# Optimization experiments

Measured on AMD Instinct MI355X. Metric: run time of the kernel, lower is better.

Reference implementation:

```python
import jax, jax.numpy as jnp
import numpy as np

H = 64   # hidden size
V = 29   # vocab / feature size
SOS = 27 # start-token index set to 1 in the initial one-hot


def _cell(x, h, c, Wih, Whh, bih, bhh):
    # PyTorch LSTMCell gate order: i, f, g, o
    g = x @ Wih.T + h @ Whh.T + bih + bhh
    i, f, gg, o = jnp.split(g, 4, axis=-1)
    c = jax.nn.sigmoid(f) * c + jax.nn.sigmoid(i) * jnp.tanh(gg)
    h = jax.nn.sigmoid(o) * jnp.tanh(c)
    return h, c


def setup_inputs() -> dict:
    key = jax.random.key(0)
    ks = iter(jax.random.split(key, 32))
    T, B = 1024, 512
    def p(shape, scale=0.05):
        return jax.random.normal(next(ks), shape, dtype=jnp.float32) * scale
    inp = {"input_seq": jax.random.normal(next(ks), (T, B, V), dtype=jnp.float32)}
    inp.update(
        enc_Wih0=p((4 * H, V)), enc_Whh0=p((4 * H, H)), enc_bih0=p((4 * H,)), enc_bhh0=p((4 * H,)),
        enc_Wih1=p((4 * H, H)), enc_Whh1=p((4 * H, H)), enc_bih1=p((4 * H,)), enc_bhh1=p((4 * H,)),
        d1_Wih=p((4 * H, V)), d1_Whh=p((4 * H, H)), d1_bih=p((4 * H,)), d1_bhh=p((4 * H,)),
        d2_Wih=p((4 * H, H)), d2_Whh=p((4 * H, H)), d2_bih=p((4 * H,)), d2_bhh=p((4 * H,)),
        cls_W=p((V, H)), cls_b=p((V,)),
    )
    return inp


def reference(input_seq, enc_Wih0, enc_Whh0, enc_bih0, enc_bhh0,
              enc_Wih1, enc_Whh1, enc_bih1, enc_bhh1,
              d1_Wih, d1_Whh, d1_bih, d1_bhh,
              d2_Wih, d2_Whh, d2_bih, d2_bhh,
              cls_W, cls_b):
    T, B, _ = input_seq.shape
    dt = input_seq.dtype
    z = jnp.zeros((B, H), dt)

    def layer(x_seq, Wih, Whh, bih, bhh):
        def step(carry, x):
            h, c = _cell(x, carry[0], carry[1], Wih, Whh, bih, bhh)
            return (h, c), h
        (h, c), ys = jax.lax.scan(step, (z, z), x_seq)
        return ys, h, c

    # 2-layer encoder LSTM with zero initial state
    y1, _, _ = layer(input_seq, enc_Wih0, enc_Whh0, enc_bih0, enc_bhh0)
    _, h1, c1 = layer(y1, enc_Wih1, enc_Whh1, enc_bih1, enc_bhh1)  # top-layer final (h, c)

    let0 = jnp.zeros((B, V), dt).at[:, SOS].set(1.0)

    def dec_step(carry, _):
        h1, c1, h2, c2, let = carry
        h1, c1 = _cell(let, h1, c1, d1_Wih, d1_Whh, d1_bih, d1_bhh)
        h2, c2 = _cell(h1, h2, c2, d2_Wih, d2_Whh, d2_bih, d2_bhh)
        pred = h2 @ cls_W.T + cls_b  # [B, V]
        idx = jnp.argmax(pred, axis=-1)  # [B]
        # Faithful to original bug: sets column idx[b] to 1 for ALL rows, for each b
        let = jnp.zeros((B, V), pred.dtype).at[:, idx].set(1.0)
        return (h1, c1, h2, c2, let), pred

    _, outputs = jax.lax.scan(dec_step, (h1, c1, z, z, let0), None, length=T)
    return outputs  # [T, B, V]
```

## Files before the change

kernel.cpp:

```cpp
#include <hip/hip_runtime.h>
#include <math.h>

#define TSTEPS 1024
#define BATCH  512
#define HID    64
#define VOC    29
#define SOS    27
#define MASK29 0x1FFFFFFFu

#define ENC_BLOCKS 256
#define DEC_BLOCKS 256
#define NTHREADS   512
#define WMAX       16

__device__ __forceinline__ float frcp(float x){ return __builtin_amdgcn_rcpf(x); }
__device__ __forceinline__ float sigmf(float x){ return frcp(1.0f + __expf(-x)); }
__device__ __forceinline__ float tanhfast(float x){ return 1.0f - 2.0f*frcp(1.0f + __expf(2.0f*x)); }

__global__ __attribute__((amdgpu_flat_work_group_size(NTHREADS,NTHREADS), amdgpu_waves_per_eu(2,2)))
void enc_kernel(const float* __restrict__ x,
                const float* __restrict__ Wih0, const float* __restrict__ Whh0,
                const float* __restrict__ bih0, const float* __restrict__ bhh0,
                const float* __restrict__ Wih1, const float* __restrict__ Whh1,
                const float* __restrict__ bih1, const float* __restrict__ bhh1,
                float* __restrict__ h1g, float* __restrict__ c1g)
{
  const int tid = threadIdx.x;
  const int b0  = blockIdx.x * 2;
  const bool g0 = tid < 256;
  const int  r  = g0 ? tid : (tid-256);

  __shared__ __align__(16) float xs[2][32];
  __shared__ __align__(16) float h0s[2][HID], h1s[2][HID];
  __shared__ __align__(16) float gA[2][256], gB[2][256];

  float wh[64], w2[64];
  if (g0){
    #pragma unroll
    for (int k=0;k<64;k++) wh[k] = Whh0[r*64+k];
    #pragma unroll
    for (int k=0;k<29;k++) w2[k] = Wih0[r*29+k];
    #pragma unroll
    for (int k=29;k<64;k++) w2[k] = 0.f;
  } else {
    #pragma unroll
    for (int k=0;k<64;k++){ wh[k] = Whh1[r*64+k]; w2[k] = Wih1[r*64+k]; }
  }
  const float bias = g0 ? (bih0[r]+bhh0[r]) : (bih1[r]+bhh1[r]);

  float creg = 0.f;
  if (tid < 128){ int u=tid>>6,k=tid&63; h0s[u][k]=0.f; h1s[u][k]=0.f; }

  const int pidx = tid - 448;
  const bool pf  = (pidx >= 0) && (pidx < 2*VOC);
  const int prow = pf ? (pidx/VOC) : 0;
  const int pcol = pf ? (pidx%VOC) : 0;
  if (pf) xs[prow][pcol] = x[(size_t)(b0+prow)*VOC + pcol];
  __syncthreads();

  for (int t=0;t<=TSTEPS;t++){
    float xv = 0.f;
    if (pf && t+1 < TSTEPS)
      xv = x[(size_t)(t+1)*BATCH*VOC + (size_t)(b0+prow)*VOC + pcol];

    if (g0){
      if (t < TSTEPS){
        #pragma unroll
        for (int u=0;u<2;u++){
          float a0=bias,a1=0.f,a2=0.f,a3=0.f;
          const float4* xv4 = (const float4*)xs[u];
          #pragma unroll
          for (int c=0;c<7;c++){
            float4 q=xv4[c];
            a0=fmaf(q.x,w2[4*c+0],a0); a1=fmaf(q.y,w2[4*c+1],a1);
            a2=fmaf(q.z,w2[4*c+2],a2); a3=fmaf(q.w,w2[4*c+3],a3);
          }
          a0=fmaf(xs[u][28],w2[28],a0);
          const float4* h4=(const float4*)h0s[u];
          #pragma unroll
          for (int c=0;c<16;c++){
            float4 q=h4[c];
            a0=fmaf(q.x,wh[4*c+0],a0); a1=fmaf(q.y,wh[4*c+1],a1);
            a2=fmaf(q.z,wh[4*c+2],a2); a3=fmaf(q.w,wh[4*c+3],a3);
          }
          gA[u][r]=(a0+a1)+(a2+a3);
        }
      }
    } else {
      if (t >= 1){
        #pragma unroll
        for (int u=0;u<2;u++){
          float a0=bias,a1=0.f,a2=0.f,a3=0.f;
          const float4* i4=(const float4*)h0s[u];
          const float4* h4=(const float4*)h1s[u];
          #pragma unroll
          for (int c=0;c<16;c++){
            float4 q=i4[c], w=h4[c];
            a0=fmaf(q.x,w2[4*c+0],a0); a1=fmaf(q.y,w2[4*c+1],a1);
            a2=fmaf(q.z,w2[4*c+2],a2); a3=fmaf(q.w,w2[4*c+3],a3);
            a0=fmaf(w.x,wh[4*c+0],a0); a1=fmaf(w.y,wh[4*c+1],a1);
            a2=fmaf(w.z,wh[4*c+2],a2); a3=fmaf(w.w,wh[4*c+3],a3);
          }
          gB[u][r]=(a0+a1)+(a2+a3);
        }
      }
    }
    __syncthreads();
    if (tid < 128){
      if (t < TSTEPS){
        int u=tid>>6,k=tid&63;
        float ig=gA[u][k],fg=gA[u][64+k],gg=gA[u][128+k],og=gA[u][192+k];
        float c=sigmf(fg)*creg + sigmf(ig)*tanhfast(gg);
        creg=c; h0s[u][k]=sigmf(og)*tanhfast(c);
      }
    } else if (tid < 384){
      if (t >= 1){
        int tt=tid-256,u=tt>>6,k=tt&63;
        float ig=gB[u][k],fg=gB[u][64+k],gg=gB[u][128+k],og=gB[u][192+k];
        float c=sigmf(fg)*creg + sigmf(ig)*tanhfast(gg);
        creg=c; h1s[u][k]=sigmf(og)*tanhfast(c);
      }
    }
    if (pf && t+1 < TSTEPS) xs[prow][pcol] = xv;
    __syncthreads();
  }

  if (tid >= 256 && tid < 384){
    int tt=tid-256,u=tt>>6,k=tt&63;
    h1g[(b0+u)*HID+k]=h1s[u][k];
    c1g[(b0+u)*HID+k]=creg;
  }
}

__global__ __attribute__((amdgpu_flat_work_group_size(NTHREADS,NTHREADS), amdgpu_waves_per_eu(2,2)))
void dec_kernel(const float* __restrict__ h1gp, const float* __restrict__ c1gp,
                const float* __restrict__ W1ih, const float* __restrict__ W1hh,
                const float* __restrict__ b1ih, const float* __restrict__ b1hh,
                const float* __restrict__ W2ih, const float* __restrict__ W2hh,
                const float* __restrict__ b2ih, const float* __restrict__ b2hh,
                const float* __restrict__ clsW, const float* __restrict__ clsb,
                float* __restrict__ out,
                unsigned long long* __restrict__ mseq)
{
  const int tid  = threadIdx.x;
  const int p    = tid & 1;
  const int r    = tid >> 1;
  const int q    = r & 3;
  const int m    = tid >> 3;
  const int g    = q*64 + m;
  const int blk  = blockIdx.x;
  const int b0   = blk * 2;

  __shared__ __align__(16) float clsW_s[VOC][68];
  __shared__ __align__(16) float clsb_s[32];
  __shared__ __align__(16) float h1s[2][2][HID], h2s[2][2][HID];
  __shared__ __align__(16) float h1ck[WMAX][2][HID], c1ck[WMAX][2][HID];
  __shared__ __align__(16) float h2ck[WMAX][2][HID], c2ck[WMAX][2][HID];
  __shared__ unsigned u_lds[WMAX];

  for (int i=tid;i<VOC*HID;i+=NTHREADS) clsW_s[i/HID][i%HID] = clsW[i];
  if (tid<VOC) clsb_s[tid]=clsb[tid];

  float w1h[32], w2i[32], w2h[32], wi1c[15];
  #pragma unroll
  for (int k=0;k<32;k++){
    w1h[k]=W1hh[g*HID+32*p+k];
    w2i[k]=W2ih[g*HID+32*p+k];
    w2h[k]=W2hh[g*HID+32*p+k];
  }
  const int cbase = p ? 15 : 0;
  const int cn    = p ? 14 : 15;
  #pragma unroll
  for (int j=0;j<15;j++) wi1c[j] = (j<cn) ? W1ih[g*VOC+cbase+j] : 0.f;
  const float biasg = p ? 0.f : (b1ih[g]+b1hh[g]);
  const float bias2 = p ? 0.f : (b2ih[g]+b2hh[g]);

  float c1r[2], c2r[2];
  c1r[0]=c1gp[(b0+0)*HID+m]; c1r[1]=c1gp[(b0+1)*HID+m];
  c2r[0]=0.f; c2r[1]=0.f;
  if (tid<128){
    int u=tid>>6,k=tid&63;
    h1s[0][u][k]=h1gp[(b0+u)*HID+k];
    h2s[0][u][k]=0.f;
  }
  __syncthreads();

  unsigned F = 1u<<SOS;
  int f = 0;
  unsigned rr = 0;
  int Wcur = 4, streak = 0;
  int pb = 0;

  while (f < TSTEPS){
    const int Wr = (TSTEPS - f < Wcur) ? (TSTEPS - f) : Wcur;
    const unsigned tag = rr + 1u;
    unsigned long long* __restrict__ mrow = mseq + (size_t)(rr&1u)*(WMAX*256);

    if (tid < Wr) u_lds[tid] = 0u;

    float it0 = biasg;
    #pragma unroll
    for (int jj=0;jj<15;jj++) it0 += ((F>>(cbase+jj))&1u) ? wi1c[jj] : 0.f;

    for (int j=0;j<Wr;j++){
      float h1n[2];
      #pragma unroll
      for (int u=0;u<2;u++){
        float a0=it0,a1=0.f,a2=0.f,a3=0.f;
        const float4* h4=(const float4*)(&h1s[pb][u][32*p]);
        #pragma unroll
        for (int c=0;c<8;c++){
          float4 qv=h4[c];
          a0=fmaf(qv.x,w1h[4*c+0],a0); a1=fmaf(qv.y,w1h[4*c+1],a1);
          a2=fmaf(qv.z,w1h[4*c+2],a2); a3=fmaf(qv.w,w1h[4*c+3],a3);
        }
        float v=(a0+a1)+(a2+a3);
        v += __shfl_xor(v,1);
        float x2=__shfl_xor(v,2), x4=__shfl_xor(v,4), x6=__shfl_xor(v,6);
        float ig = q==0?v : q==1?x2 : q==2?x4 : x6;
        float fg = q==1?v : q==0?x2 : q==3?x4 : x6;
        float gg = q==2?v : q==3?x2 : q==0?x4 : x6;
        float og = q==3?v : q==2?x2 : q==1?x4 : x6;
        float c = sigmf(fg)*c1r[u] + sigmf(ig)*tanhfast(gg);
        c1r[u]=c; h1n[u]=sigmf(og)*tanhfast(c);
      }
      if ((tid&7)==0){
        h1s[pb^1][0][m]=h1n[0]; h1s[pb^1][1][m]=h1n[1];
        h1ck[j][0][m]=h1n[0];   h1ck[j][1][m]=h1n[1];
        c1ck[j][0][m]=c1r[0];   c1ck[j][1][m]=c1r[1];
      }
      __syncthreads();

      float h2n[2];
      #pragma unroll
      for (int u=0;u<2;u++){
        float a0=bias2,a1=0.f,a2=0.f,a3=0.f;
        const float4* i4=(const float4*)(&h1s[pb^1][u][32*p]);
        const float4* h4=(const float4*)(&h2s[pb][u][32*p]);
        #pragma unroll
        for (int c=0;c<8;c++){
          float4 qv=i4[c], wv=h4[c];
          a0=fmaf(qv.x,w2i[4*c+0],a0); a1=fmaf(qv.y,w2i[4*c+1],a1);
          a2=fmaf(qv.z,w2i[4*c+2],a2); a3=fmaf(qv.w,w2i[4*c+3],a3);
          a0=fmaf(wv.x,w2h[4*c+0],a0); a1=fmaf(wv.y,w2h[4*c+1],a1);
          a2=fmaf(wv.z,w2h[4*c+2],a2); a3=fmaf(wv.w,w2h[4*c+3],a3);
        }
        float v=(a0+a1)+(a2+a3);
        v += __shfl_xor(v,1);
        float x2=__shfl_xor(v,2), x4=__shfl_xor(v,4), x6=__shfl_xor(v,6);
        float ig = q==0?v : q==1?x2 : q==2?x4 : x6;
        float fg = q==1?v : q==0?x2 : q==3?x4 : x6;
        float gg = q==2?v : q==3?x2 : q==0?x4 : x6;
        float og = q==3?v : q==2?x2 : q==1?x4 : x6;
        float c = sigmf(fg)*c2r[u] + sigmf(ig)*tanhfast(gg);
        c2r[u]=c; h2n[u]=sigmf(og)*tanhfast(c);
      }
      if ((tid&7)==0){
        h2s[pb^1][0][m]=h2n[0]; h2s[pb^1][1][m]=h2n[1];
        h2ck[j][0][m]=h2n[0];   h2ck[j][1][m]=h2n[1];
        c2ck[j][0][m]=c2r[0];   c2ck[j][1][m]=c2r[1];
      }
      __syncthreads();

      if (tid<64){
        const int s = f + j;
        int row=tid>>5, v=tid&31;
        float pv = -INFINITY;
        if (v<VOC){
          float a0=clsb_s[v],a1=0.f,a2=0.f,a3=0.f;
          const float4* h4=(const float4*)h2s[pb^1][row];
          #pragma unroll
          for (int c=0;c<16;c++){
            float4 qv=h4[c];
            a0=fmaf(qv.x,clsW_s[v][4*c+0],a0); a1=fmaf(qv.y,clsW_s[v][4*c+1],a1);
            a2=fmaf(qv.z,clsW_s[v][4*c+2],a2); a3=fmaf(qv.w,clsW_s[v][4*c+3],a3);
          }
          pv=(a0+a1)+(a2+a3);
          out[((size_t)s*BATCH + (size_t)(b0+row))*VOC + v]=pv;
        }
        int ix=v;
        #pragma unroll
        for (int off=16; off>0; off>>=1){
          float ov=__shfl_xor(pv,off);
          int   oi=__shfl_xor(ix,off);
          if (ov>pv || (ov==pv && oi<ix)){ pv=ov; ix=oi; }
        }
        unsigned bit = 1u<<ix;
        unsigned mb  = bit | __shfl_xor(bit,32);
        if (tid==0)
          __hip_atomic_store(&mrow[j*256+blk],
                             ((unsigned long long)tag<<32) | (unsigned long long)mb,
                             __ATOMIC_RELAXED, __HIP_MEMORY_SCOPE_AGENT);
      }
      pb ^= 1;
    }

    for (int w=tid; w<Wr*256; w+=NTHREADS){
      const int jj = w>>8, bb = w&255;
      unsigned long long vv;
      do {
        vv = __hip_atomic_load(&mrow[jj*256+bb], __ATOMIC_RELAXED, __HIP_MEMORY_SCOPE_AGENT);
      } while ((unsigned)(vv>>32) != tag);
      unsigned um = (unsigned)vv & MASK29;
      um |= __shfl_xor(um,1);  um |= __shfl_xor(um,2);  um |= __shfl_xor(um,4);
      um |= __shfl_xor(um,8);  um |= __shfl_xor(um,16); um |= __shfl_xor(um,32);
      if ((tid&63)==0) atomicOr(&u_lds[jj], um);
    }
    __syncthreads();

    int jstar = Wr;
    for (int jj=1;jj<Wr;jj++){ if (u_lds[jj-1]!=F){ jstar=jj; break; } }

    if (jstar==Wr){
      F = u_lds[Wr-1]; f += Wr; rr++;
      streak++;
      if (streak>=2 && Wcur<WMAX) Wcur*=2;
    } else {
      const int jm = jstar-1;
      c1r[0]=c1ck[jm][0][m]; c1r[1]=c1ck[jm][1][m];
      c2r[0]=c2ck[jm][0][m]; c2r[1]=c2ck[jm][1][m];
      if (tid<128){
        int u=tid>>6,k=tid&63;
        h1s[0][u][k]=h1ck[jm][u][k];
        h2s[0][u][k]=h2ck[jm][u][k];
      }
      pb = 0;
      F = u_lds[jm]; f += jstar; rr++;
      streak = 0; Wcur = jstar;
    }
    __syncthreads();
  }
}

extern "C" void kernel_launch(void* const* d_in, const int* in_sizes, int n_in,
                              void* d_out, int out_size, void* d_ws, size_t ws_size,
                              hipStream_t stream)
{
  const float* x     = (const float*)d_in[0];
  const float* eWih0 = (const float*)d_in[1];
  const float* eWhh0 = (const float*)d_in[2];
  const float* ebih0 = (const float*)d_in[3];
  const float* ebhh0 = (const float*)d_in[4];
  const float* eWih1 = (const float*)d_in[5];
  const float* eWhh1 = (const float*)d_in[6];
  const float* ebih1 = (const float*)d_in[7];
  const float* ebhh1 = (const float*)d_in[8];
  const float* d1Wih = (const float*)d_in[9];
  const float* d1Whh = (const float*)d_in[10];
  const float* d1bih = (const float*)d_in[11];
  const float* d1bhh = (const float*)d_in[12];
  const float* d2Wih = (const float*)d_in[13];
  const float* d2Whh = (const float*)d_in[14];
  const float* d2bih = (const float*)d_in[15];
  const float* d2bhh = (const float*)d_in[16];
  const float* clsW  = (const float*)d_in[17];
  const float* clsb  = (const float*)d_in[18];
  float* out = (float*)d_out;

  float* h1g = (float*)d_ws;
  float* c1g = h1g + BATCH*HID;
  unsigned long long* mseq =
      (unsigned long long*)((char*)d_ws + (size_t)(2*BATCH*HID)*sizeof(float));

  hipMemsetAsync(mseq, 0, (size_t)2*WMAX*256*sizeof(unsigned long long), stream);

  enc_kernel<<<ENC_BLOCKS, NTHREADS, 0, stream>>>(
      x, eWih0,eWhh0,ebih0,ebhh0, eWih1,eWhh1,ebih1,ebhh1, h1g,c1g);

  void* args[] = { (void*)&h1g, (void*)&c1g,
                   (void*)&d1Wih,(void*)&d1Whh,(void*)&d1bih,(void*)&d1bhh,
                   (void*)&d2Wih,(void*)&d2Whh,(void*)&d2bih,(void*)&d2bhh,
                   (void*)&clsW,(void*)&clsb,(void*)&out,
                   (void*)&mseq };
  hipLaunchCooperativeKernel((void*)dec_kernel, dim3(DEC_BLOCKS), dim3(NTHREADS),
                             args, 0, stream);
}
```

Baseline: 4.874 ms.

## Fuse encoder gate activation into matvec threads via shuffles, double-buffer state

The encoder kernel remaps threads so each quad of lanes holds the i/f/g/o rows for one hidden unit, exchanges the gate pre-activations with warp shuffles, and computes the cell update in place. This drops the gate LDS arrays and one of the two barriers per timestep. h and x buffers are double-buffered so the next step's reads don't race with writes. Every thread now evaluates the activation transcendentals redundantly, and the cell state is replicated four times.

```diff
diff --git a/kernel.cpp b/kernel.cpp
--- a/kernel.cpp
+++ b/kernel.cpp
@@ -28,107 +28,113 @@
   const int tid = threadIdx.x;
   const int b0  = blockIdx.x * 2;
   const bool g0 = tid < 256;
-  const int  r  = g0 ? tid : (tid-256);
-
-  __shared__ __align__(16) float xs[2][32];
-  __shared__ __align__(16) float h0s[2][HID], h1s[2][HID];
-  __shared__ __align__(16) float gA[2][256], gB[2][256];
-
-  float wh[64], w2[64];
+  const int  t2 = g0 ? tid : (tid-256);
+  const int  q  = t2 & 3;
+  const int  m  = t2 >> 2;
+  const int  g  = q*64 + m;
+
+  __shared__ __align__(16) float xs[2][2][32];
+  __shared__ __align__(16) float h0s[2][2][HID], h1s[2][2][HID];
+
+  float wa[64], wb[64];
+  float bias;
   if (g0){
     #pragma unroll
-    for (int k=0;k<64;k++) wh[k] = Whh0[r*64+k];
-    #pragma unroll
-    for (int k=0;k<29;k++) w2[k] = Wih0[r*29+k];
-    #pragma unroll
-    for (int k=29;k<64;k++) w2[k] = 0.f;
+    for (int k=0;k<29;k++) wa[k]=Wih0[g*29+k];
+    #pragma unroll
+    for (int k=29;k<64;k++) wa[k]=0.f;
+    #pragma unroll
+    for (int k=0;k<64;k++) wb[k]=Whh0[g*64+k];
+    bias = bih0[g]+bhh0[g];
   } else {
     #pragma unroll
-    for (int k=0;k<64;k++){ wh[k] = Whh1[r*64+k]; w2[k] = Wih1[r*64+k]; }
-  }
-  const float bias = g0 ? (bih0[r]+bhh0[r]) : (bih1[r]+bhh1[r]);
-
-  float creg = 0.f;
-  if (tid < 128){ int u=tid>>6,k=tid&63; h0s[u][k]=0.f; h1s[u][k]=0.f; }
-
-  const int pidx = tid - 448;
-  const bool pf  = (pidx >= 0) && (pidx < 2*VOC);
-  const int prow = pf ? (pidx/VOC) : 0;
-  const int pcol = pf ? (pidx%VOC) : 0;
-  if (pf) xs[prow][pcol] = x[(size_t)(b0+prow)*VOC + pcol];
+    for (int k=0;k<64;k++){ wa[k]=Wih1[g*64+k]; wb[k]=Whh1[g*64+k]; }
+    bias = bih1[g]+bhh1[g];
+  }
+
+  float creg[2]={0.f,0.f};
+  float hn[2]={0.f,0.f};
+
+  if (tid<256){ ((float*)h0s)[tid]=0.f; ((float*)h1s)[tid]=0.f; }
+  const int lrow = tid/29, lcol = tid - lrow*29;
+  const bool ldr = g0 && (tid<58);
+  if (ldr) xs[0][lrow][lcol] = x[(size_t)(b0+lrow)*VOC + lcol];
   __syncthreads();
 
+  int pb=0;
+  const bool q0=(q==0), q1=(q==1), q2=(q==2), q3=(q==3);
+
   for (int t=0;t<=TSTEPS;t++){
-    float xv = 0.f;
-    if (pf && t+1 < TSTEPS)
-      xv = x[(size_t)(t+1)*BATCH*VOC + (size_t)(b0+prow)*VOC + pcol];
+    float xv=0.f;
+    if (ldr && t+1<TSTEPS)
+      xv = x[(size_t)(t+1)*BATCH*VOC + (size_t)(b0+lrow)*VOC + lcol];
 
     if (g0){
-      if (t < TSTEPS){
+      if (t<TSTEPS){
         #pragma unroll
         for (int u=0;u<2;u++){
           float a0=bias,a1=0.f,a2=0.f,a3=0.f;
-          const float4* xv4 = (const float4*)xs[u];
+          const float4* xv4=(const float4*)xs[pb][u];
           #pragma unroll
           for (int c=0;c<7;c++){
-            float4 q=xv4[c];
-            a0=fmaf(q.x,w2[4*c+0],a0); a1=fmaf(q.y,w2[4*c+1],a1);
-            a2=fmaf(q.z,w2[4*c+2],a2); a3=fmaf(q.w,w2[4*c+3],a3);
+            float4 qv=xv4[c];
+            a0=fmaf(qv.x,wa[4*c+0],a0); a1=fmaf(qv.y,wa[4*c+1],a1);
+            a2=fmaf(qv.z,wa[4*c+2],a2); a3=fmaf(qv.w,wa[4*c+3],a3);
           }
-          a0=fmaf(xs[u][28],w2[28],a0);
-          const float4* h4=(const float4*)h0s[u];
+          a0=fmaf(xs[pb][u][28],wa[28],a0);
+          const float4* h4=(const float4*)h0s[pb][u];
           #pragma unroll
           for (int c=0;c<16;c++){
-            float4 q=h4[c];
-            a0=fmaf(q.x,wh[4*c+0],a0); a1=fmaf(q.y,wh[4*c+1],a1);
-            a2=fmaf(q.z,wh[4*c+2],a2); a3=fmaf(q.w,wh[4*c+3],a3);
+            float4 qv=h4[c];
+            a0=fmaf(qv.x,wb[4*c+0],a0); a1=fmaf(qv.y,wb[4*c+1],a1);
+            a2=fmaf(qv.z,wb[4*c+2],a2); a3=fmaf(qv.w,wb[4*c+3],a3);
           }
-          gA[u][r]=(a0+a1)+(a2+a3);
-        }
+          float v=(a0+a1)+(a2+a3);
+          float s1=__shfl_xor(v,1), s2=__shfl_xor(v,2), s3=__shfl_xor(v,3);
+          float ig = q0?v : q1?s1 : q2?s2 : s3;
+          float fg = q1?v : q0?s1 : q3?s2 : s3;
+          float gg = q2?v : q3?s1 : q0?s2 : s3;
+          float og = q3?v : q2?s1 : q1?s2 : s3;
+          float c = sigmf(fg)*creg[u] + sigmf(ig)*tanhfast(gg);
+          creg[u]=c; hn[u]=sigmf(og)*tanhfast(c);
+        }
+        if (q0){ h0s[pb^1][0][m]=hn[0]; h0s[pb^1][1][m]=hn[1]; }
       }
     } else {
-      if (t >= 1){
+      if (t>=1){
         #pragma unroll
         for (int u=0;u<2;u++){
           float a0=bias,a1=0.f,a2=0.f,a3=0.f;
-          const float4* i4=(const float4*)h0s[u];
-          const float4* h4=(const float4*)h1s[u];
+          const float4* i4=(const float4*)h0s[pb][u];
+          const float4* h4=(const float4*)h1s[pb][u];
           #pragma unroll
           for (int c=0;c<16;c++){
-            float4 q=i4[c], w=h4[c];
-            a0=fmaf(q.x,w2[4*c+0],a0); a1=fmaf(q.y,w2[4*c+1],a1);
-            a2=fmaf(q.z,w2[4*c+2],a2); a3=fmaf(q.w,w2[4*c+3],a3);
-            a0=fmaf(w.x,wh[4*c+0],a0); a1=fmaf(w.y,wh[4*c+1],a1);
-            a2=fmaf(w.z,wh[4*c+2],a2); a3=fmaf(w.w,wh[4*c+3],a3);
+            float4 qv=i4[c], wv=h4[c];
+            a0=fmaf(qv.x,wa[4*c+0],a0); a1=fmaf(qv.y,wa[4*c+1],a1);
+            a2=fmaf(qv.z,wa[4*c+2],a2); a3=fmaf(qv.w,wa[4*c+3],a3);
+            a0=fmaf(wv.x,wb[4*c+0],a0); a1=fmaf(wv.y,wb[4*c+1],a1);
+            a2=fmaf(wv.z,wb[4*c+2],a2); a3=fmaf(wv.w,wb[4*c+3],a3);
           }
-          gB[u][r]=(a0+a1)+(a2+a3);
-        }
+          float v=(a0+a1)+(a2+a3);
+          float s1=__shfl_xor(v,1), s2=__shfl_xor(v,2), s3=__shfl_xor(v,3);
+          float ig = q0?v : q1?s1 : q2?s2 : s3;
+          float fg = q1?v : q0?s1 : q3?s2 : s3;
+          float gg = q2?v : q3?s1 : q0?s2 : s3;
+          float og = q3?v : q2?s1 : q1?s2 : s3;
+          float c = sigmf(fg)*creg[u] + sigmf(ig)*tanhfast(gg);
+          creg[u]=c; hn[u]=sigmf(og)*tanhfast(c);
+        }
+        if (q0){ h1s[pb^1][0][m]=hn[0]; h1s[pb^1][1][m]=hn[1]; }
       }
     }
+    if (ldr && t+1<TSTEPS) xs[pb^1][lrow][lcol]=xv;
     __syncthreads();
-    if (tid < 128){
-      if (t < TSTEPS){
-        int u=tid>>6,k=tid&63;
-        float ig=gA[u][k],fg=gA[u][64+k],gg=gA[u][128+k],og=gA[u][192+k];
-        float c=sigmf(fg)*creg + sigmf(ig)*tanhfast(gg);
-        creg=c; h0s[u][k]=sigmf(og)*tanhfast(c);
-      }
-    } else if (tid < 384){
-      if (t >= 1){
-        int tt=tid-256,u=tt>>6,k=tt&63;
-        float ig=gB[u][k],fg=gB[u][64+k],gg=gB[u][128+k],og=gB[u][192+k];
-        float c=sigmf(fg)*creg + sigmf(ig)*tanhfast(gg);
-        creg=c; h1s[u][k]=sigmf(og)*tanhfast(c);
-      }
-    }
-    if (pf && t+1 < TSTEPS) xs[prow][pcol] = xv;
-    __syncthreads();
-  }
-
-  if (tid >= 256 && tid < 384){
-    int tt=tid-256,u=tt>>6,k=tt&63;
-    h1g[(b0+u)*HID+k]=h1s[u][k];
-    c1g[(b0+u)*HID+k]=creg;
+    pb^=1;
+  }
+
+  if (!g0 && q0){
+    h1g[(b0+0)*HID+m]=hn[0];   h1g[(b0+1)*HID+m]=hn[1];
+    c1g[(b0+0)*HID+m]=creg[0]; c1g[(b0+1)*HID+m]=creg[1];
   }
 }
 
@@ -312,7 +318,8 @@
     for (int jj=1;jj<Wr;jj++){ if (u_lds[jj-1]!=F){ jstar=jj; break; } }
 
     if (jstar==Wr){
-      F = u_lds[Wr-1]; f += Wr; rr++;
+      F = u_lds[Wr-1];
+      f += Wr; rr++;
       streak++;
       if (streak>=2 && Wcur<WMAX) Wcur*=2;
     } else {
```

Result: slower. 7.707 ms (+58.1%).

## Fuse encoder into cooperative decoder kernel and batch input prefetch in chunks

Applied to the files above, without the earlier changes.

Merges the encoder and decoder into one cooperative kernel. Each block runs its encoder batch rows, keeps the final h/c in shared memory and goes straight into decoding, which removes the second launch and the global round-trip of encoder state. Input loads are now prefetched eight timesteps at a time into a double-buffered shared array instead of one step per iteration. The speculative decode window now grows only after four clean rounds instead of two. Risks include higher shared-memory and register pressure in the fused kernel and a less aggressive window growth policy.

```diff
diff --git a/kernel.cpp b/kernel.cpp
--- a/kernel.cpp
+++ b/kernel.cpp
@@ -8,132 +8,21 @@
 #define SOS    27
 #define MASK29 0x1FFFFFFFu
 
-#define ENC_BLOCKS 256
-#define DEC_BLOCKS 256
-#define NTHREADS   512
-#define WMAX       16
+#define NBLOCKS  256
+#define NTHREADS 512
+#define WMAX     16
+#define XCH      8
 
 __device__ __forceinline__ float frcp(float x){ return __builtin_amdgcn_rcpf(x); }
 __device__ __forceinline__ float sigmf(float x){ return frcp(1.0f + __expf(-x)); }
 __device__ __forceinline__ float tanhfast(float x){ return 1.0f - 2.0f*frcp(1.0f + __expf(2.0f*x)); }
 
 __global__ __attribute__((amdgpu_flat_work_group_size(NTHREADS,NTHREADS), amdgpu_waves_per_eu(2,2)))
-void enc_kernel(const float* __restrict__ x,
+void s2s_kernel(const float* __restrict__ x,
                 const float* __restrict__ Wih0, const float* __restrict__ Whh0,
                 const float* __restrict__ bih0, const float* __restrict__ bhh0,
                 const float* __restrict__ Wih1, const float* __restrict__ Whh1,
                 const float* __restrict__ bih1, const float* __restrict__ bhh1,
-                float* __restrict__ h1g, float* __restrict__ c1g)
-{
-  const int tid = threadIdx.x;
-  const int b0  = blockIdx.x * 2;
-  const bool g0 = tid < 256;
-  const int  r  = g0 ? tid : (tid-256);
-
-  __shared__ __align__(16) float xs[2][32];
-  __shared__ __align__(16) float h0s[2][HID], h1s[2][HID];
-  __shared__ __align__(16) float gA[2][256], gB[2][256];
-
-  float wh[64], w2[64];
-  if (g0){
-    #pragma unroll
-    for (int k=0;k<64;k++) wh[k] = Whh0[r*64+k];
-    #pragma unroll
-    for (int k=0;k<29;k++) w2[k] = Wih0[r*29+k];
-    #pragma unroll
-    for (int k=29;k<64;k++) w2[k] = 0.f;
-  } else {
-    #pragma unroll
-    for (int k=0;k<64;k++){ wh[k] = Whh1[r*64+k]; w2[k] = Wih1[r*64+k]; }
-  }
-  const float bias = g0 ? (bih0[r]+bhh0[r]) : (bih1[r]+bhh1[r]);
-
-  float creg = 0.f;
-  if (tid < 128){ int u=tid>>6,k=tid&63; h0s[u][k]=0.f; h1s[u][k]=0.f; }
-
-  const int pidx = tid - 448;
-  const bool pf  = (pidx >= 0) && (pidx < 2*VOC);
-  const int prow = pf ? (pidx/VOC) : 0;
-  const int pcol = pf ? (pidx%VOC) : 0;
-  if (pf) xs[prow][pcol] = x[(size_t)(b0+prow)*VOC + pcol];
-  __syncthreads();
-
-  for (int t=0;t<=TSTEPS;t++){
-    float xv = 0.f;
-    if (pf && t+1 < TSTEPS)
-      xv = x[(size_t)(t+1)*BATCH*VOC + (size_t)(b0+prow)*VOC + pcol];
-
-    if (g0){
-      if (t < TSTEPS){
-        #pragma unroll
-        for (int u=0;u<2;u++){
-          float a0=bias,a1=0.f,a2=0.f,a3=0.f;
-          const float4* xv4 = (const float4*)xs[u];
-          #pragma unroll
-          for (int c=0;c<7;c++){
-            float4 q=xv4[c];
-            a0=fmaf(q.x,w2[4*c+0],a0); a1=fmaf(q.y,w2[4*c+1],a1);
-            a2=fmaf(q.z,w2[4*c+2],a2); a3=fmaf(q.w,w2[4*c+3],a3);
-          }
-          a0=fmaf(xs[u][28],w2[28],a0);
-          const float4* h4=(const float4*)h0s[u];
-          #pragma unroll
-          for (int c=0;c<16;c++){
-            float4 q=h4[c];
-            a0=fmaf(q.x,wh[4*c+0],a0); a1=fmaf(q.y,wh[4*c+1],a1);
-            a2=fmaf(q.z,wh[4*c+2],a2); a3=fmaf(q.w,wh[4*c+3],a3);
-          }
-          gA[u][r]=(a0+a1)+(a2+a3);
-        }
-      }
-    } else {
-      if (t >= 1){
-        #pragma unroll
-        for (int u=0;u<2;u++){
-          float a0=bias,a1=0.f,a2=0.f,a3=0.f;
-          const float4* i4=(const float4*)h0s[u];
-          const float4* h4=(const float4*)h1s[u];
-          #pragma unroll
-          for (int c=0;c<16;c++){
-            float4 q=i4[c], w=h4[c];
-            a0=fmaf(q.x,w2[4*c+0],a0); a1=fmaf(q.y,w2[4*c+1],a1);
-            a2=fmaf(q.z,w2[4*c+2],a2); a3=fmaf(q.w,w2[4*c+3],a3);
-            a0=fmaf(w.x,wh[4*c+0],a0); a1=fmaf(w.y,wh[4*c+1],a1);
-            a2=fmaf(w.z,wh[4*c+2],a2); a3=fmaf(w.w,wh[4*c+3],a3);
-          }
-          gB[u][r]=(a0+a1)+(a2+a3);
-        }
-      }
-    }
-    __syncthreads();
-    if (tid < 128){
-      if (t < TSTEPS){
-        int u=tid>>6,k=tid&63;
-        float ig=gA[u][k],fg=gA[u][64+k],gg=gA[u][128+k],og=gA[u][192+k];
-        float c=sigmf(fg)*creg + sigmf(ig)*tanhfast(gg);
-        creg=c; h0s[u][k]=sigmf(og)*tanhfast(c);
-      }
-    } else if (tid < 384){
-      if (t >= 1){
-        int tt=tid-256,u=tt>>6,k=tt&63;
-        float ig=gB[u][k],fg=gB[u][64+k],gg=gB[u][128+k],og=gB[u][192+k];
-        float c=sigmf(fg)*creg + sigmf(ig)*tanhfast(gg);
-        creg=c; h1s[u][k]=sigmf(og)*tanhfast(c);
-      }
-    }
-    if (pf && t+1 < TSTEPS) xs[prow][pcol] = xv;
-    __syncthreads();
-  }
-
-  if (tid >= 256 && tid < 384){
-    int tt=tid-256,u=tt>>6,k=tt&63;
-    h1g[(b0+u)*HID+k]=h1s[u][k];
-    c1g[(b0+u)*HID+k]=creg;
-  }
-}
-
-__global__ __attribute__((amdgpu_flat_work_group_size(NTHREADS,NTHREADS), amdgpu_waves_per_eu(2,2)))
-void dec_kernel(const float* __restrict__ h1gp, const float* __restrict__ c1gp,
                 const float* __restrict__ W1ih, const float* __restrict__ W1hh,
                 const float* __restrict__ b1ih, const float* __restrict__ b1hh,
                 const float* __restrict__ W2ih, const float* __restrict__ W2hh,
@@ -142,15 +31,14 @@
                 float* __restrict__ out,
                 unsigned long long* __restrict__ mseq)
 {
-  const int tid  = threadIdx.x;
-  const int p    = tid & 1;
-  const int r    = tid >> 1;
-  const int q    = r & 3;
-  const int m    = tid >> 3;
-  const int g    = q*64 + m;
-  const int blk  = blockIdx.x;
-  const int b0   = blk * 2;
-
+  const int tid = threadIdx.x;
+  const int blk = blockIdx.x;
+  const int b0  = blk * 2;
+
+  __shared__ __align__(16) float xs[2][XCH][2][32];
+  __shared__ __align__(16) float eh0[2][HID], eh1[2][HID];
+  __shared__ __align__(16) float gA[2][256], gB[2][256];
+  __shared__ __align__(16) float c1buf[2][HID];
   __shared__ __align__(16) float clsW_s[VOC][68];
   __shared__ __align__(16) float clsb_s[32];
   __shared__ __align__(16) float h1s[2][2][HID], h2s[2][2][HID];
@@ -161,40 +49,153 @@
   for (int i=tid;i<VOC*HID;i+=NTHREADS) clsW_s[i/HID][i%HID] = clsW[i];
   if (tid<VOC) clsb_s[tid]=clsb[tid];
 
+  {
+    const bool g0 = tid < 256;
+    const int  r  = g0 ? tid : (tid-256);
+
+    float wh[64], w2[64];
+    if (g0){
+      #pragma unroll
+      for (int k=0;k<64;k++) wh[k] = Whh0[r*64+k];
+      #pragma unroll
+      for (int k=0;k<29;k++) w2[k] = Wih0[r*29+k];
+      #pragma unroll
+      for (int k=29;k<64;k++) w2[k] = 0.f;
+    } else {
+      #pragma unroll
+      for (int k=0;k<64;k++){ wh[k] = Whh1[r*64+k]; w2[k] = Wih1[r*64+k]; }
+    }
+    const float bias = g0 ? (bih0[r]+bhh0[r]) : (bih1[r]+bhh1[r]);
+
+    float creg = 0.f;
+    if (tid < 128){ int u=tid>>6,k=tid&63; eh0[u][k]=0.f; eh1[u][k]=0.f; }
+
+    const bool ldr  = tid < 2*VOC*XCH;
+    const int  toff = ldr ? tid/(2*VOC) : 0;
+    const int  lrem = ldr ? tid%(2*VOC) : 0;
+    const int  lrow = lrem/VOC, lcol = lrem%VOC;
+    if (ldr) xs[0][toff][lrow][lcol] =
+        x[(size_t)toff*BATCH*VOC + (size_t)(b0+lrow)*VOC + lcol];
+    __syncthreads();
+
+    float xv = 0.f;
+    for (int t=0;t<=TSTEPS;t++){
+      if (((t&(XCH-1))==0) && ldr){
+        const int tl = t + XCH + toff;
+        xv = (tl < TSTEPS)
+           ? x[(size_t)tl*BATCH*VOC + (size_t)(b0+lrow)*VOC + lcol] : 0.f;
+      }
+
+      if (g0){
+        if (t < TSTEPS){
+          const int par = (t>>3)&1, sl = t&7;
+          #pragma unroll
+          for (int u=0;u<2;u++){
+            float a0=bias,a1=0.f,a2=0.f,a3=0.f;
+            const float4* xv4 = (const float4*)xs[par][sl][u];
+            #pragma unroll
+            for (int c=0;c<7;c++){
+              float4 q=xv4[c];
+              a0=fmaf(q.x,w2[4*c+0],a0); a1=fmaf(q.y,w2[4*c+1],a1);
+              a2=fmaf(q.z,w2[4*c+2],a2); a3=fmaf(q.w,w2[4*c+3],a3);
+            }
+            a0=fmaf(xs[par][sl][u][28],w2[28],a0);
+            const float4* h4=(const float4*)eh0[u];
+            #pragma unroll
+            for (int c=0;c<16;c++){
+              float4 q=h4[c];
+              a0=fmaf(q.x,wh[4*c+0],a0); a1=fmaf(q.y,wh[4*c+1],a1);
+              a2=fmaf(q.z,wh[4*c+2],a2); a3=fmaf(q.w,wh[4*c+3],a3);
+            }
+            gA[u][r]=(a0+a1)+(a2+a3);
+          }
+        }
+      } else {
+        if (t >= 1){
+          #pragma unroll
+          for (int u=0;u<2;u++){
+            float a0=bias,a1=0.f,a2=0.f,a3=0.f;
+            const float4* i4=(const float4*)eh0[u];
+            const float4* h4=(const float4*)eh1[u];
+            #pragma unroll
+            for (int c=0;c<16;c++){
+              float4 q=i4[c], w=h4[c];
+              a0=fmaf(q.x,w2[4*c+0],a0); a1=fmaf(q.y,w2[4*c+1],a1);
+              a2=fmaf(q.z,w2[4*c+2],a2); a3=fmaf(q.w,w2[4*c+3],a3);
+              a0=fmaf(w.x,wh[4*c+0],a0); a1=fmaf(w.y,wh[4*c+1],a1);
+              a2=fmaf(w.z,wh[4*c+2],a2); a3=fmaf(w.w,wh[4*c+3],a3);
+            }
+            gB[u][r]=(a0+a1)+(a2+a3);
+          }
+        }
+      }
+      __syncthreads();
+      if (tid < 128){
+        if (t < TSTEPS){
+          int u=tid>>6,k=tid&63;
+          float ig=gA[u][k],fg=gA[u][64+k],gg=gA[u][128+k],og=gA[u][192+k];
+          float c=sigmf(fg)*creg + sigmf(ig)*tanhfast(gg);
+          creg=c; eh0[u][k]=sigmf(og)*tanhfast(c);
+        }
+      } else if (tid >= 256 && tid < 384){
+        if (t >= 1){
+          int tt=tid-256,u=tt>>6,k=tt&63;
+          float ig=gB[u][k],fg=gB[u][64+k],gg=gB[u][128+k],og=gB[u][192+k];
+          float c=sigmf(fg)*creg + sigmf(ig)*tanhfast(gg);
+          creg=c; eh1[u][k]=sigmf(og)*tanhfast(c);
+        }
+      }
+      if (((t&(XCH-1))==(XCH-1)) && ldr)
+        xs[((t>>3)+1)&1][toff][lrow][lcol] = xv;
+      __syncthreads();
+    }
+
+    if (tid >= 256 && tid < 384){
+      int tt=tid-256,u=tt>>6,k=tt&63;
+      c1buf[u][k]=creg;
+    }
+  }
+  __syncthreads();
+
+  const int pd = tid & 1;
+  const int qd = (tid >> 1) & 3;
+  const int md = tid >> 3;
+  const int gd = qd*64 + md;
+
   float w1h[32], w2i[32], w2h[32], wi1c[15];
   #pragma unroll
   for (int k=0;k<32;k++){
-    w1h[k]=W1hh[g*HID+32*p+k];
-    w2i[k]=W2ih[g*HID+32*p+k];
-    w2h[k]=W2hh[g*HID+32*p+k];
+    w1h[k]=W1hh[gd*HID+32*pd+k];
+    w2i[k]=W2ih[gd*HID+32*pd+k];
+    w2h[k]=W2hh[gd*HID+32*pd+k];
   }
-  const int cbase = p ? 15 : 0;
-  const int cn    = p ? 14 : 15;
+  const int cbase = pd ? 15 : 0;
+  const int cn    = pd ? 14 : 15;
   #pragma unroll
-  for (int j=0;j<15;j++) wi1c[j] = (j<cn) ? W1ih[g*VOC+cbase+j] : 0.f;
-  const float biasg = p ? 0.f : (b1ih[g]+b1hh[g]);
-  const float bias2 = p ? 0.f : (b2ih[g]+b2hh[g]);
+  for (int j=0;j<15;j++) wi1c[j] = (j<cn) ? W1ih[gd*VOC+cbase+j] : 0.f;
+  const float biasg = pd ? 0.f : (b1ih[gd]+b1hh[gd]);
+  const float bias2 = pd ? 0.f : (b2ih[gd]+b2hh[gd]);
 
   float c1r[2], c2r[2];
-  c1r[0]=c1gp[(b0+0)*HID+m]; c1r[1]=c1gp[(b0+1)*HID+m];
+  c1r[0]=c1buf[0][md]; c1r[1]=c1buf[1][md];
   c2r[0]=0.f; c2r[1]=0.f;
   if (tid<128){
     int u=tid>>6,k=tid&63;
-    h1s[0][u][k]=h1gp[(b0+u)*HID+k];
+    h1s[0][u][k]=eh1[u][k];
     h2s[0][u][k]=0.f;
   }
   __syncthreads();
 
   unsigned F = 1u<<SOS;
   int f = 0;
-  unsigned rr = 0;
+  unsigned rnd = 0;
   int Wcur = 4, streak = 0;
   int pb = 0;
 
   while (f < TSTEPS){
     const int Wr = (TSTEPS - f < Wcur) ? (TSTEPS - f) : Wcur;
-    const unsigned tag = rr + 1u;
-    unsigned long long* __restrict__ mrow = mseq + (size_t)(rr&1u)*(WMAX*256);
+    const unsigned tag = rnd + 1u;
+    unsigned long long* __restrict__ mrow = mseq + (size_t)(rnd&1u)*(WMAX*256);
 
     if (tid < Wr) u_lds[tid] = 0u;
 
@@ -207,7 +208,7 @@
       #pragma unroll
       for (int u=0;u<2;u++){
         float a0=it0,a1=0.f,a2=0.f,a3=0.f;
-        const float4* h4=(const float4*)(&h1s[pb][u][32*p]);
+        const float4* h4=(const float4*)(&h1s[pb][u][32*pd]);
         #pragma unroll
         for (int c=0;c<8;c++){
           float4 qv=h4[c];
@@ -217,17 +218,17 @@
         float v=(a0+a1)+(a2+a3);
         v += __shfl_xor(v,1);
         float x2=__shfl_xor(v,2), x4=__shfl_xor(v,4), x6=__shfl_xor(v,6);
-        float ig = q==0?v : q==1?x2 : q==2?x4 : x6;
-        float fg = q==1?v : q==0?x2 : q==3?x4 : x6;
-        float gg = q==2?v : q==3?x2 : q==0?x4 : x6;
-        float og = q==3?v : q==2?x2 : q==1?x4 : x6;
+        float ig = qd==0?v : qd==1?x2 : qd==2?x4 : x6;
+        float fg = qd==1?v : qd==0?x2 : qd==3?x4 : x6;
+        float gg = qd==2?v : qd==3?x2 : qd==0?x4 : x6;
+        float og = qd==3?v : qd==2?x2 : qd==1?x4 : x6;
         float c = sigmf(fg)*c1r[u] + sigmf(ig)*tanhfast(gg);
         c1r[u]=c; h1n[u]=sigmf(og)*tanhfast(c);
       }
       if ((tid&7)==0){
-        h1s[pb^1][0][m]=h1n[0]; h1s[pb^1][1][m]=h1n[1];
-        h1ck[j][0][m]=h1n[0];   h1ck[j][1][m]=h1n[1];
-        c1ck[j][0][m]=c1r[0];   c1ck[j][1][m]=c1r[1];
+        h1s[pb^1][0][md]=h1n[0]; h1s[pb^1][1][md]=h1n[1];
+        h1ck[j][0][md]=h1n[0];   h1ck[j][1][md]=h1n[1];
+        c1ck[j][0][md]=c1r[0];   c1ck[j][1][md]=c1r[1];
       }
       __syncthreads();
 
@@ -235,8 +236,8 @@
       #pragma unroll
       for (int u=0;u<2;u++){
         float a0=bias2,a1=0.f,a2=0.f,a3=0.f;
-        const float4* i4=(const float4*)(&h1s[pb^1][u][32*p]);
-        const float4* h4=(const float4*)(&h2s[pb][u][32*p]);
+        const float4* i4=(const float4*)(&h1s[pb^1][u][32*pd]);
+        const float4* h4=(const float4*)(&h2s[pb][u][32*pd]);
         #pragma unroll
         for (int c=0;c<8;c++){
           float4 qv=i4[c], wv=h4[c];
@@ -248,17 +249,17 @@
         float v=(a0+a1)+(a2+a3);
         v += __shfl_xor(v,1);
         float x2=__shfl_xor(v,2), x4=__shfl_xor(v,4), x6=__shfl_xor(v,6);
-        float ig = q==0?v : q==1?x2 : q==2?x4 : x6;
-        float fg = q==1?v : q==0?x2 : q==3?x4 : x6;
-        float gg = q==2?v : q==3?x2 : q==0?x4 : x6;
-        float og = q==3?v : q==2?x2 : q==1?x4 : x6;
+        float ig = qd==0?v : qd==1?x2 : qd==2?x4 : x6;
+        float fg = qd==1?v : qd==0?x2 : qd==3?x4 : x6;
+        float gg = qd==2?v : qd==3?x2 : qd==0?x4 : x6;
+        float og = qd==3?v : qd==2?x2 : qd==1?x4 : x6;
         float c = sigmf(fg)*c2r[u] + sigmf(ig)*tanhfast(gg);
         c2r[u]=c; h2n[u]=sigmf(og)*tanhfast(c);
       }
       if ((tid&7)==0){
-        h2s[pb^1][0][m]=h2n[0]; h2s[pb^1][1][m]=h2n[1];
-        h2ck[j][0][m]=h2n[0];   h2ck[j][1][m]=h2n[1];
-        c2ck[j][0][m]=c2r[0];   c2ck[j][1][m]=c2r[1];
+        h2s[pb^1][0][md]=h2n[0]; h2s[pb^1][1][md]=h2n[1];
+        h2ck[j][0][md]=h2n[0];   h2ck[j][1][md]=h2n[1];
+        c2ck[j][0][md]=c2r[0];   c2ck[j][1][md]=c2r[1];
       }
       __syncthreads();
 
@@ -312,20 +313,21 @@
     for (int jj=1;jj<Wr;jj++){ if (u_lds[jj-1]!=F){ jstar=jj; break; } }
 
     if (jstar==Wr){
-      F = u_lds[Wr-1]; f += Wr; rr++;
+      F = u_lds[Wr-1];
+      f += Wr; rnd++;
       streak++;
-      if (streak>=2 && Wcur<WMAX) Wcur*=2;
+      if (streak>=4 && Wcur<WMAX) Wcur*=2;
     } else {
       const int jm = jstar-1;
-      c1r[0]=c1ck[jm][0][m]; c1r[1]=c1ck[jm][1][m];
-      c2r[0]=c2ck[jm][0][m]; c2r[1]=c2ck[jm][1][m];
+      c1r[0]=c1ck[jm][0][md]; c1r[1]=c1ck[jm][1][md];
+      c2r[0]=c2ck[jm][0][md]; c2r[1]=c2ck[jm][1][md];
       if (tid<128){
         int u=tid>>6,k=tid&63;
         h1s[0][u][k]=h1ck[jm][u][k];
         h2s[0][u][k]=h2ck[jm][u][k];
       }
       pb = 0;
-      F = u_lds[jm]; f += jstar; rr++;
+      F = u_lds[jm]; f += jstar; rnd++;
       streak = 0; Wcur = jstar;
     }
     __syncthreads();
@@ -357,21 +359,15 @@
   const float* clsb  = (const float*)d_in[18];
   float* out = (float*)d_out;
 
-  float* h1g = (float*)d_ws;
-  float* c1g = h1g + BATCH*HID;
-  unsigned long long* mseq =
-      (unsigned long long*)((char*)d_ws + (size_t)(2*BATCH*HID)*sizeof(float));
-
+  unsigned long long* mseq = (unsigned long long*)d_ws;
   hipMemsetAsync(mseq, 0, (size_t)2*WMAX*256*sizeof(unsigned long long), stream);
 
-  enc_kernel<<<ENC_BLOCKS, NTHREADS, 0, stream>>>(
-      x, eWih0,eWhh0,ebih0,ebhh0, eWih1,eWhh1,ebih1,ebhh1, h1g,c1g);
-
-  void* args[] = { (void*)&h1g, (void*)&c1g,
+  void* args[] = { (void*)&x,
+                   (void*)&eWih0,(void*)&eWhh0,(void*)&ebih0,(void*)&ebhh0,
+                   (void*)&eWih1,(void*)&eWhh1,(void*)&ebih1,(void*)&ebhh1,
                    (void*)&d1Wih,(void*)&d1Whh,(void*)&d1bih,(void*)&d1bhh,
                    (void*)&d2Wih,(void*)&d2Whh,(void*)&d2bih,(void*)&d2bhh,
-                   (void*)&clsW,(void*)&clsb,(void*)&out,
-                   (void*)&mseq };
-  hipLaunchCooperativeKernel((void*)dec_kernel, dim3(DEC_BLOCKS), dim3(NTHREADS),
+                   (void*)&clsW,(void*)&clsb,(void*)&out,(void*)&mseq };
+  hipLaunchCooperativeKernel((void*)s2s_kernel, dim3(NBLOCKS), dim3(NTHREADS),
                              args, 0, stream);
 }
```

Measured after the change: 4.892 ms. No clear change (+0.4%).
